# Optimization experiments

Hardware: AMD Instinct MI355X
Metric: run time of the kernel (lower is better)

Reference implementation:

```python
import jax, jax.numpy as jnp
import numpy as np

IN_FEATURES = 4096
OUT_FEATURES = 4096
PACKED_IN = (IN_FEATURES + 3) // 4  # 1024


def _unpack_ternary(packed, scale, original_in_features):
    # packed: (O, P) uint8; each byte holds 4 two-bit fields encoding {-1,0,+1} as {0,1,2}
    p = packed.astype(jnp.uint8)
    fields = jnp.stack(
        [p & 3, (p >> 2) & 3, (p >> 4) & 3, (p >> 6) & 3], axis=-1
    )  # (O, P, 4)
    unpacked = fields.reshape(packed.shape[0], -1)[:, :original_in_features]
    decoded = unpacked.astype(scale.dtype) - 1.0  # back to {-1,0,+1}
    return decoded * scale  # per-output-channel scale, (O, IN)


def setup_inputs() -> dict:
    key = jax.random.key(0)
    k_x, k_w, k_s, k_b = jax.random.split(key, 4)
    x = jax.random.normal(k_x, (4, 2048, IN_FEATURES), dtype=jnp.float32)
    # sample ternary codes {0,1,2} per 2-bit field, then pack 4 per byte
    fields = jax.random.randint(k_w, (OUT_FEATURES, PACKED_IN, 4), 0, 3).astype(jnp.uint8)
    packed_weight = (
        fields[..., 0]
        | (fields[..., 1] << 2)
        | (fields[..., 2] << 4)
        | (fields[..., 3] << 6)
    )  # (O, P) uint8
    scale = jax.random.uniform(k_s, (OUT_FEATURES, 1), dtype=jnp.float32, minval=0.01, maxval=0.1)
    bias = jax.random.normal(k_b, (OUT_FEATURES,), dtype=jnp.float32)
    return {"x": x, "packed_weight": packed_weight, "scale": scale, "bias": bias}


def reference(x, packed_weight, scale, bias):
    weight = _unpack_ternary(packed_weight, scale, IN_FEATURES)  # (O, IN) fp32
    # F.linear: x @ W.T + b
    return jnp.einsum("bsi,oi->bso", x, weight) + bias
```

## Files before the change

kernel.cpp:

```cpp
#include <hip/hip_runtime.h>
#include <hip/hip_bf16.h>
#include <stdint.h>

#define M_TOT 8192
#define N_TOT 4096
#define K_TOT 4096
#define PACKED_K 1024

typedef __attribute__((ext_vector_type(4))) float f32x4;
typedef __attribute__((ext_vector_type(4))) int i32x4;
typedef __attribute__((ext_vector_type(16))) int i32x16;
typedef __attribute__((ext_vector_type(4))) unsigned int u32x4;

typedef const __attribute__((address_space(1))) void* gas_cptr;
typedef __attribute__((address_space(3))) void* las_ptr;

#define SX (6.0f / 127.0f)
#define SX_INV (127.0f / 6.0f)

__device__ __forceinline__ void gload_lds16(const void* g, void* l) {
    __builtin_amdgcn_global_load_lds((gas_cptr)g, (las_ptr)l, 16, 0, 0);
}

__global__ void detect_i32(const uint32_t* __restrict__ pw, uint32_t* __restrict__ flag) {
    if (threadIdx.x == 0) {
        uint32_t small = 1u;
        for (int i = 0; i < 64; ++i)
            if (pw[i] > 255u) small = 0u;
        *flag = small;
    }
}


__device__ __forceinline__ uint32_t q8pack(f32x4 v) {
    int a = (int)rintf(fminf(fmaxf(v.x * SX_INV, -127.f), 127.f));
    int b = (int)rintf(fminf(fmaxf(v.y * SX_INV, -127.f), 127.f));
    int c = (int)rintf(fminf(fmaxf(v.z * SX_INV, -127.f), 127.f));
    int d = (int)rintf(fminf(fmaxf(v.w * SX_INV, -127.f), 127.f));
    return (uint32_t)(a & 0xFF) | ((uint32_t)(b & 0xFF) << 8)
         | ((uint32_t)(c & 0xFF) << 16) | ((uint32_t)(d & 0xFF) << 24);
}

__global__ void quant_x_tiled(const float* __restrict__ x,
                              int8_t* __restrict__ aq, int ngran) {
    int stride = gridDim.x * blockDim.x;
    for (int g = blockIdx.x * blockDim.x + threadIdx.x; g < ngran; g += stride) {
        const int mb = g >> 16;
        const int w16 = g & 65535;
        const int kt = w16 >> 10;
        const int w = w16 & 1023;
        const int kstep = w >> 9;
        const int rb = (w >> 6) & 7;
        const int kslot = (w >> 5) & 1;
        const int rl = w & 31;
        const int row = mb * 256 + rb * 32 + rl;
        const int col = kt * 64 + kstep * 32 + kslot * 16;
        const f32x4* src = (const f32x4*)(x + (size_t)row * K_TOT + col);
        uint32_t w0 = q8pack(src[0]);
        uint32_t w1 = q8pack(src[1]);
        uint32_t w2 = q8pack(src[2]);
        uint32_t w3 = q8pack(src[3]);
        *(u32x4*)(aq + (size_t)g * 16) = (u32x4){w0, w1, w2, w3};
    }
}

__global__ void unpack_w_tiled(const uint8_t* __restrict__ pw,
                               int8_t* __restrict__ bq,
                               const uint32_t* __restrict__ flag, int ngran) {
    const uint32_t i32mode = *flag;
    int stride = gridDim.x * blockDim.x;
    for (int g = blockIdx.x * blockDim.x + threadIdx.x; g < ngran; g += stride) {
        const int nb = g >> 16;
        const int w16 = g & 65535;
        const int kt = w16 >> 10;
        const int w = w16 & 1023;
        const int kstep = w >> 9;
        const int rb = (w >> 6) & 7;
        const int kslot = (w >> 5) & 1;
        const int rl = w & 31;
        const int row = nb * 256 + rb * 32 + rl;
        const int pidx = row * PACKED_K + kt * 16 + kstep * 8 + kslot * 4;
        uint32_t p;
        if (i32mode) {
            const uint32_t* p32 = (const uint32_t*)pw;
            uint32_t b0 = p32[pidx + 0] & 0xFFu;
            uint32_t b1 = p32[pidx + 1] & 0xFFu;
            uint32_t b2 = p32[pidx + 2] & 0xFFu;
            uint32_t b3 = p32[pidx + 3] & 0xFFu;
            p = b0 | (b1 << 8) | (b2 << 16) | (b3 << 24);
        } else {
            p = *(const uint32_t*)(pw + pidx);
        }
        uint32_t o[4];
#pragma unroll
        for (int i = 0; i < 4; ++i) {
            uint32_t b = (p >> (8 * i)) & 0xFFu;
            uint32_t f0 = b & 3u, f1 = (b >> 2) & 3u, f2 = (b >> 4) & 3u, f3 = b >> 6;
            o[i] = ((f0 - 1u) & 0xFFu) | (((f1 - 1u) & 0xFFu) << 8)
                 | (((f2 - 1u) & 0xFFu) << 16) | (((f3 - 1u) & 0xFFu) << 24);
        }
        *(u32x4*)(bq + (size_t)g * 16) = (u32x4){o[0], o[1], o[2], o[3]};
    }
}

__global__ __launch_bounds__(512, 2) void gemm_tern_i8(
        const int8_t* __restrict__ Aq,
        const int8_t* __restrict__ Bq,
        const float* __restrict__ scale,
        const float* __restrict__ bias,
        float* __restrict__ out) {
    __shared__ uint8_t lds[65536];
    uint8_t* ldsA = lds;
    uint8_t* ldsB = lds + 32768;

    const int tid  = threadIdx.x;
    const int lane = tid & 63;
    const int wid  = tid >> 6;
    const int wm   = wid >> 2;
    const int wn   = wid & 3;

    const int wg  = blockIdx.x;
    const int cpx = gridDim.x >> 3;
    const int swz = (wg & 7) * cpx + (wg >> 3);
    const int mblk = swz >> 4;
    const int nblk = swz & 15;
    const int m0  = mblk * 256;
    const int n0  = nblk * 256;

    const int8_t* Abase = Aq + (size_t)mblk * 1048576;
    const int8_t* Bbase = Bq + (size_t)nblk * 1048576;

#define STAGE(t, db) do {                                                             \
        const int8_t* sa = Abase + (size_t)(t) * 16384 + (tid << 4);                  \
        const int8_t* sb = Bbase + (size_t)(t) * 16384 + (tid << 4);                  \
        gload_lds16(sa,        ldsA + (db) * 16384 + (tid << 4));                     \
        gload_lds16(sa + 8192, ldsA + (db) * 16384 + 8192 + (tid << 4));              \
        gload_lds16(sb,        ldsB + (db) * 16384 + (tid << 4));                     \
        gload_lds16(sb + 8192, ldsB + (db) * 16384 + 8192 + (tid << 4));              \
    } while (0)

#define RD_A(mf, ks, db) (*(const i32x4*)(ldsA + (db) * 16384 + (ks) * 8192          \
                              + (wm * 4 + (mf)) * 1024 + (lane << 4)))
#define RD_B(nf, ks, db) (*(const i32x4*)(ldsB + (db) * 16384 + (ks) * 8192          \
                              + (wn * 2 + (nf)) * 1024 + (lane << 4)))

#define BAR()        __builtin_amdgcn_s_barrier()
#define SCHEDBAR()   __builtin_amdgcn_sched_barrier(0)
#define WAIT_LGKM6() asm volatile("s_waitcnt lgkmcnt(6)" ::: "memory")
#define WAIT_LGKM0() asm volatile("s_waitcnt lgkmcnt(0)" ::: "memory")
#define WAIT_VM0()   asm volatile("s_waitcnt vmcnt(0)" ::: "memory")

#define MFMA_I8(a, b, c) __builtin_amdgcn_mfma_i32_32x32x32_i8(a, b, c, 0, 0, 0)

#define KTILE(t, DB)                                                                  \
    a0k0 = RD_A(0, 0, DB); a1k0 = RD_A(1, 0, DB);                                     \
    a2k0 = RD_A(2, 0, DB); a3k0 = RD_A(3, 0, DB);                                     \
    b0k0 = RD_B(0, 0, DB); b1k0 = RD_B(1, 0, DB);                                     \
    a0k1 = RD_A(0, 1, DB); a1k1 = RD_A(1, 1, DB);                                     \
    a2k1 = RD_A(2, 1, DB); a3k1 = RD_A(3, 1, DB);                                     \
    b0k1 = RD_B(0, 1, DB); b1k1 = RD_B(1, 1, DB);                                     \
    if ((t) + 1 < NT) STAGE((t) + 1, 1 - (DB));                                       \
    WAIT_LGKM6(); SCHEDBAR();                                                         \
    __builtin_amdgcn_s_setprio(1);                                                    \
    acc00 = MFMA_I8(a0k0, b0k0, acc00);  acc01 = MFMA_I8(a0k0, b1k0, acc01);          \
    acc10 = MFMA_I8(a1k0, b0k0, acc10);  acc11 = MFMA_I8(a1k0, b1k0, acc11);          \
    acc20 = MFMA_I8(a2k0, b0k0, acc20);  acc21 = MFMA_I8(a2k0, b1k0, acc21);          \
    acc30 = MFMA_I8(a3k0, b0k0, acc30);  acc31 = MFMA_I8(a3k0, b1k0, acc31);          \
    __builtin_amdgcn_s_setprio(0);                                                    \
    WAIT_LGKM0(); SCHEDBAR();                                                         \
    __builtin_amdgcn_s_setprio(1);                                                    \
    acc00 = MFMA_I8(a0k1, b0k1, acc00);  acc01 = MFMA_I8(a0k1, b1k1, acc01);          \
    acc10 = MFMA_I8(a1k1, b0k1, acc10);  acc11 = MFMA_I8(a1k1, b1k1, acc11);          \
    acc20 = MFMA_I8(a2k1, b0k1, acc20);  acc21 = MFMA_I8(a2k1, b1k1, acc21);          \
    acc30 = MFMA_I8(a3k1, b0k1, acc30);  acc31 = MFMA_I8(a3k1, b1k1, acc31);          \
    __builtin_amdgcn_s_setprio(0);                                                    \
    WAIT_VM0();                                                                       \
    BAR();

    i32x16 acc00 = {0}, acc01 = {0}, acc10 = {0}, acc11 = {0};
    i32x16 acc20 = {0}, acc21 = {0}, acc30 = {0}, acc31 = {0};
#pragma unroll
    for (int j = 0; j < 16; ++j) {
        acc00[j] = 0; acc01[j] = 0; acc10[j] = 0; acc11[j] = 0;
        acc20[j] = 0; acc21[j] = 0; acc30[j] = 0; acc31[j] = 0;
    }

    const int NT = K_TOT / 64;

    STAGE(0, 0);
    WAIT_VM0();
    BAR();

    i32x4 a0k0, a1k0, a2k0, a3k0, b0k0, b1k0;
    i32x4 a0k1, a1k1, a2k1, a3k1, b0k1, b1k1;

    for (int t = 0; t < NT; t += 2) {
        KTILE(t, 0);
        KTILE(t + 1, 1);
    }

    const int rl    = lane & 31;
    const int rbase = (lane >> 5) << 2;
#pragma unroll
    for (int nf = 0; nf < 2; ++nf) {
        const int col = n0 + wn * 64 + nf * 32 + rl;
        const float fs = SX * scale[col];
        const float bv = bias[col];
#pragma unroll
        for (int mf = 0; mf < 4; ++mf) {
            const i32x16 a = (mf == 0) ? (nf == 0 ? acc00 : acc01)
                           : (mf == 1) ? (nf == 0 ? acc10 : acc11)
                           : (mf == 2) ? (nf == 0 ? acc20 : acc21)
                                       : (nf == 0 ? acc30 : acc31);
#pragma unroll
            for (int j = 0; j < 16; ++j) {
                const int row = m0 + wm * 128 + mf * 32 + (j & 3) + 8 * (j >> 2) + rbase;
                out[(size_t)row * N_TOT + col] = (float)a[j] * fs + bv;
            }
        }
    }
#undef STAGE
#undef RD_A
#undef RD_B
#undef BAR
#undef SCHEDBAR
#undef WAIT_LGKM6
#undef WAIT_LGKM0
#undef WAIT_VM0
#undef MFMA_I8
#undef KTILE
}

__global__ void naive_tern(const float* __restrict__ x,
                           const uint8_t* __restrict__ pw,
                           const float* __restrict__ scale,
                           const float* __restrict__ bias,
                           float* __restrict__ out) {
    const int n = blockIdx.x * blockDim.x + threadIdx.x;
    const int m = blockIdx.y;
    const uint32_t* p32 = (const uint32_t*)pw;
    bool i32mode = true;
    for (int i = 0; i < 64; ++i)
        if (p32[i] > 255u) { i32mode = false; break; }
    const float* xr = x + (size_t)m * K_TOT;
    float acc = 0.f;
    if (i32mode) {
        const uint32_t* wr = p32 + (size_t)n * PACKED_K;
        for (int p = 0; p < PACKED_K; ++p) {
            uint32_t b = wr[p] & 0xFFu;
            acc += xr[4 * p + 0] * (float)((int)(b & 3u) - 1);
            acc += xr[4 * p + 1] * (float)((int)((b >> 2) & 3u) - 1);
            acc += xr[4 * p + 2] * (float)((int)((b >> 4) & 3u) - 1);
            acc += xr[4 * p + 3] * (float)((int)((b >> 6) & 3u) - 1);
        }
    } else {
        const uint8_t* wr = pw + (size_t)n * PACKED_K;
        for (int p = 0; p < PACKED_K; ++p) {
            uint32_t b = wr[p];
            acc += xr[4 * p + 0] * (float)((int)(b & 3u) - 1);
            acc += xr[4 * p + 1] * (float)((int)((b >> 2) & 3u) - 1);
            acc += xr[4 * p + 2] * (float)((int)((b >> 4) & 3u) - 1);
            acc += xr[4 * p + 3] * (float)((int)((b >> 6) & 3u) - 1);
        }
    }
    out[(size_t)m * N_TOT + n] = acc * scale[n] + bias[n];
}

extern "C" void kernel_launch(void* const* d_in, const int* in_sizes, int n_in,
                              void* d_out, int out_size, void* d_ws, size_t ws_size,
                              hipStream_t stream) {
    const float*   x     = (const float*)d_in[0];
    const uint8_t* pw    = (const uint8_t*)d_in[1];
    const float*   scale = (const float*)d_in[2];
    const float*   bias  = (const float*)d_in[3];
    float*         out   = (float*)d_out;

    const size_t A_BYTES = (size_t)M_TOT * K_TOT;
    const size_t B_BYTES = (size_t)N_TOT * K_TOT;
    const size_t NEED    = A_BYTES + B_BYTES + 64;

    if (ws_size >= NEED) {
        int8_t*   Aq   = (int8_t*)d_ws;
        int8_t*   Bq   = (int8_t*)((uint8_t*)d_ws + A_BYTES);
        uint32_t* flag = (uint32_t*)((uint8_t*)d_ws + A_BYTES + B_BYTES);
        detect_i32<<<1, 64, 0, stream>>>((const uint32_t*)pw, flag);
        unpack_w_tiled<<<2048, 256, 0, stream>>>(pw, Bq, flag, (int)(B_BYTES / 16));
        quant_x_tiled<<<2048, 256, 0, stream>>>(x, Aq, (int)(A_BYTES / 16));
        gemm_tern_i8<<<(M_TOT / 256) * (N_TOT / 256), 512, 0, stream>>>(Aq, Bq, scale, bias, out);
    } else {
        dim3 grid(N_TOT / 256, M_TOT);
        naive_tern<<<grid, 256, 0, stream>>>(x, pw, scale, bias, out);
    }
}
```

Baseline: 194.3 us.

## Load B fragments directly from global into registers, keep only A in LDS

The int8 GEMM stops staging the B (weight) tile through LDS. Each wave now loads its B fragments straight from global memory into double-buffered registers one K-tile ahead, which halves LDS use and removes the B LDS reads. The tile traversal is also switched to be N-major with M inner, so neighbouring workgroups share a B block, and the detect kernel uses a wave ballot instead of a serial loop. In exchange, B loads are no longer shared across the two waves that read the same B columns, which doubles B global traffic from L2. Register pressure also rises under launch_bounds(512,2).

```diff
diff --git a/kernel.cpp b/kernel.cpp
--- a/kernel.cpp
+++ b/kernel.cpp
@@ -23,12 +23,8 @@
 }
 
 __global__ void detect_i32(const uint32_t* __restrict__ pw, uint32_t* __restrict__ flag) {
-    if (threadIdx.x == 0) {
-        uint32_t small = 1u;
-        for (int i = 0; i < 64; ++i)
-            if (pw[i] > 255u) small = 0u;
-        *flag = small;
-    }
+    unsigned long long big = __ballot(pw[threadIdx.x & 63] > 255u);
+    if (threadIdx.x == 0) *flag = (big == 0ull) ? 1u : 0u;
 }
 
 
@@ -109,9 +105,7 @@
         const float* __restrict__ scale,
         const float* __restrict__ bias,
         float* __restrict__ out) {
-    __shared__ uint8_t lds[65536];
-    uint8_t* ldsA = lds;
-    uint8_t* ldsB = lds + 32768;
+    __shared__ uint8_t ldsA[32768];
 
     const int tid  = threadIdx.x;
     const int lane = tid & 63;
@@ -122,57 +116,59 @@
     const int wg  = blockIdx.x;
     const int cpx = gridDim.x >> 3;
     const int swz = (wg & 7) * cpx + (wg >> 3);
-    const int mblk = swz >> 4;
-    const int nblk = swz & 15;
+    const int nblk = swz >> 5;
+    const int mblk = swz & 31;
     const int m0  = mblk * 256;
     const int n0  = nblk * 256;
 
     const int8_t* Abase = Aq + (size_t)mblk * 1048576;
     const int8_t* Bbase = Bq + (size_t)nblk * 1048576;
-
-#define STAGE(t, db) do {                                                             \
+    const i32x4*  Bb4   = (const i32x4*)(Bbase + wn * 2048 + (lane << 4));
+
+#define STAGE_A(t, db) do {                                                           \
         const int8_t* sa = Abase + (size_t)(t) * 16384 + (tid << 4);                  \
-        const int8_t* sb = Bbase + (size_t)(t) * 16384 + (tid << 4);                  \
         gload_lds16(sa,        ldsA + (db) * 16384 + (tid << 4));                     \
         gload_lds16(sa + 8192, ldsA + (db) * 16384 + 8192 + (tid << 4));              \
-        gload_lds16(sb,        ldsB + (db) * 16384 + (tid << 4));                     \
-        gload_lds16(sb + 8192, ldsB + (db) * 16384 + 8192 + (tid << 4));              \
+    } while (0)
+
+#define LOADB(r00, r10, r01, r11, t) do {                                             \
+        const i32x4* pb = Bb4 + (size_t)(t) * 1024;                                   \
+        r00 = pb[0]; r10 = pb[64]; r01 = pb[512]; r11 = pb[576];                      \
     } while (0)
 
 #define RD_A(mf, ks, db) (*(const i32x4*)(ldsA + (db) * 16384 + (ks) * 8192          \
                               + (wm * 4 + (mf)) * 1024 + (lane << 4)))
-#define RD_B(nf, ks, db) (*(const i32x4*)(ldsB + (db) * 16384 + (ks) * 8192          \
-                              + (wn * 2 + (nf)) * 1024 + (lane << 4)))
 
 #define BAR()        __builtin_amdgcn_s_barrier()
 #define SCHEDBAR()   __builtin_amdgcn_sched_barrier(0)
-#define WAIT_LGKM6() asm volatile("s_waitcnt lgkmcnt(6)" ::: "memory")
+#define WAIT_LGKM4() asm volatile("s_waitcnt lgkmcnt(4)" ::: "memory")
 #define WAIT_LGKM0() asm volatile("s_waitcnt lgkmcnt(0)" ::: "memory")
 #define WAIT_VM0()   asm volatile("s_waitcnt vmcnt(0)" ::: "memory")
 
 #define MFMA_I8(a, b, c) __builtin_amdgcn_mfma_i32_32x32x32_i8(a, b, c, 0, 0, 0)
 
-#define KTILE(t, DB)                                                                  \
+#define KTILE(t, DB, Bc00, Bc10, Bc01, Bc11, Bn00, Bn10, Bn01, Bn11)                  \
+    if ((t) + 1 < NT) {                                                               \
+        STAGE_A((t) + 1, 1 - (DB));                                                   \
+        LOADB(Bn00, Bn10, Bn01, Bn11, (t) + 1);                                       \
+    }                                                                                 \
     a0k0 = RD_A(0, 0, DB); a1k0 = RD_A(1, 0, DB);                                     \
     a2k0 = RD_A(2, 0, DB); a3k0 = RD_A(3, 0, DB);                                     \
-    b0k0 = RD_B(0, 0, DB); b1k0 = RD_B(1, 0, DB);                                     \
     a0k1 = RD_A(0, 1, DB); a1k1 = RD_A(1, 1, DB);                                     \
     a2k1 = RD_A(2, 1, DB); a3k1 = RD_A(3, 1, DB);                                     \
-    b0k1 = RD_B(0, 1, DB); b1k1 = RD_B(1, 1, DB);                                     \
-    if ((t) + 1 < NT) STAGE((t) + 1, 1 - (DB));                                       \
-    WAIT_LGKM6(); SCHEDBAR();                                                         \
+    WAIT_LGKM4(); SCHEDBAR();                                                         \
     __builtin_amdgcn_s_setprio(1);                                                    \
-    acc00 = MFMA_I8(a0k0, b0k0, acc00);  acc01 = MFMA_I8(a0k0, b1k0, acc01);          \
-    acc10 = MFMA_I8(a1k0, b0k0, acc10);  acc11 = MFMA_I8(a1k0, b1k0, acc11);          \
-    acc20 = MFMA_I8(a2k0, b0k0, acc20);  acc21 = MFMA_I8(a2k0, b1k0, acc21);          \
-    acc30 = MFMA_I8(a3k0, b0k0, acc30);  acc31 = MFMA_I8(a3k0, b1k0, acc31);          \
+    acc00 = MFMA_I8(a0k0, Bc00, acc00);  acc01 = MFMA_I8(a0k0, Bc10, acc01);          \
+    acc10 = MFMA_I8(a1k0, Bc00, acc10);  acc11 = MFMA_I8(a1k0, Bc10, acc11);          \
+    acc20 = MFMA_I8(a2k0, Bc00, acc20);  acc21 = MFMA_I8(a2k0, Bc10, acc21);          \
+    acc30 = MFMA_I8(a3k0, Bc00, acc30);  acc31 = MFMA_I8(a3k0, Bc10, acc31);          \
     __builtin_amdgcn_s_setprio(0);                                                    \
     WAIT_LGKM0(); SCHEDBAR();                                                         \
     __builtin_amdgcn_s_setprio(1);                                                    \
-    acc00 = MFMA_I8(a0k1, b0k1, acc00);  acc01 = MFMA_I8(a0k1, b1k1, acc01);          \
-    acc10 = MFMA_I8(a1k1, b0k1, acc10);  acc11 = MFMA_I8(a1k1, b1k1, acc11);          \
-    acc20 = MFMA_I8(a2k1, b0k1, acc20);  acc21 = MFMA_I8(a2k1, b1k1, acc21);          \
-    acc30 = MFMA_I8(a3k1, b0k1, acc30);  acc31 = MFMA_I8(a3k1, b1k1, acc31);          \
+    acc00 = MFMA_I8(a0k1, Bc01, acc00);  acc01 = MFMA_I8(a0k1, Bc11, acc01);          \
+    acc10 = MFMA_I8(a1k1, Bc01, acc10);  acc11 = MFMA_I8(a1k1, Bc11, acc11);          \
+    acc20 = MFMA_I8(a2k1, Bc01, acc20);  acc21 = MFMA_I8(a2k1, Bc11, acc21);          \
+    acc30 = MFMA_I8(a3k1, Bc01, acc30);  acc31 = MFMA_I8(a3k1, Bc11, acc31);          \
     __builtin_amdgcn_s_setprio(0);                                                    \
     WAIT_VM0();                                                                       \
     BAR();
@@ -187,16 +183,19 @@
 
     const int NT = K_TOT / 64;
 
-    STAGE(0, 0);
+    i32x4 Bx00, Bx10, Bx01, Bx11, By00, By10, By01, By11;
+
+    STAGE_A(0, 0);
+    LOADB(Bx00, Bx10, Bx01, Bx11, 0);
     WAIT_VM0();
     BAR();
 
-    i32x4 a0k0, a1k0, a2k0, a3k0, b0k0, b1k0;
-    i32x4 a0k1, a1k1, a2k1, a3k1, b0k1, b1k1;
+    i32x4 a0k0, a1k0, a2k0, a3k0;
+    i32x4 a0k1, a1k1, a2k1, a3k1;
 
     for (int t = 0; t < NT; t += 2) {
-        KTILE(t, 0);
-        KTILE(t + 1, 1);
+        KTILE(t,     0, Bx00, Bx10, Bx01, Bx11, By00, By10, By01, By11);
+        KTILE(t + 1, 1, By00, By10, By01, By11, Bx00, Bx10, Bx01, Bx11);
     }
 
     const int rl    = lane & 31;
@@ -219,12 +218,12 @@
             }
         }
     }
-#undef STAGE
+#undef STAGE_A
+#undef LOADB
 #undef RD_A
-#undef RD_B
 #undef BAR
 #undef SCHEDBAR
-#undef WAIT_LGKM6
+#undef WAIT_LGKM4
 #undef WAIT_LGKM0
 #undef WAIT_VM0
 #undef MFMA_I8
```

New measurement: 210.9 us. 8.6% more time.

## Deepen int8 GEMM LDS pipeline to four stages with prefetch three tiles ahead

Applied to the files above, without the earlier changes.

The int8 ternary GEMM moves from a double-buffered LDS scheme to a four-slot ring of 32KB tiles. Global-to-LDS loads are issued three K-tiles ahead, and the wait only drains to vmcnt(8), so two tiles stay in flight instead of stalling on every load each iteration. The K loop is unrolled by four with a hand-written tail that stops staging and shrinks the wait counts. This doubles LDS per block to 128KB, which likely limits the CU to one resident 512-thread block instead of the two the launch bounds target, trading occupancy for deeper prefetch. A small secondary change replaces the serial 64-element check in detect_i32 with a wavefront ballot.

```diff
diff --git a/kernel.cpp b/kernel.cpp
--- a/kernel.cpp
+++ b/kernel.cpp
@@ -23,12 +23,8 @@
 }
 
 __global__ void detect_i32(const uint32_t* __restrict__ pw, uint32_t* __restrict__ flag) {
-    if (threadIdx.x == 0) {
-        uint32_t small = 1u;
-        for (int i = 0; i < 64; ++i)
-            if (pw[i] > 255u) small = 0u;
-        *flag = small;
-    }
+    unsigned long long big = __ballot(pw[threadIdx.x & 63] > 255u);
+    if (threadIdx.x == 0) *flag = (big == 0ull) ? 1u : 0u;
 }
 
 
@@ -109,9 +105,7 @@
         const float* __restrict__ scale,
         const float* __restrict__ bias,
         float* __restrict__ out) {
-    __shared__ uint8_t lds[65536];
-    uint8_t* ldsA = lds;
-    uint8_t* ldsB = lds + 32768;
+    __shared__ uint8_t lds[131072];
 
     const int tid  = threadIdx.x;
     const int lane = tid & 63;
@@ -133,48 +127,48 @@
 #define STAGE(t, db) do {                                                             \
         const int8_t* sa = Abase + (size_t)(t) * 16384 + (tid << 4);                  \
         const int8_t* sb = Bbase + (size_t)(t) * 16384 + (tid << 4);                  \
-        gload_lds16(sa,        ldsA + (db) * 16384 + (tid << 4));                     \
-        gload_lds16(sa + 8192, ldsA + (db) * 16384 + 8192 + (tid << 4));              \
-        gload_lds16(sb,        ldsB + (db) * 16384 + (tid << 4));                     \
-        gload_lds16(sb + 8192, ldsB + (db) * 16384 + 8192 + (tid << 4));              \
+        uint8_t* la = lds + (db) * 32768 + (tid << 4);                                \
+        gload_lds16(sa,        la);                                                   \
+        gload_lds16(sa + 8192, la + 8192);                                            \
+        gload_lds16(sb,        la + 16384);                                           \
+        gload_lds16(sb + 8192, la + 24576);                                           \
     } while (0)
 
-#define RD_A(mf, ks, db) (*(const i32x4*)(ldsA + (db) * 16384 + (ks) * 8192          \
+#define RD_A(mf, ks, db) (*(const i32x4*)(lds + (db) * 32768 + (ks) * 8192           \
                               + (wm * 4 + (mf)) * 1024 + (lane << 4)))
-#define RD_B(nf, ks, db) (*(const i32x4*)(ldsB + (db) * 16384 + (ks) * 8192          \
+#define RD_B(nf, ks, db) (*(const i32x4*)(lds + (db) * 32768 + 16384 + (ks) * 8192   \
                               + (wn * 2 + (nf)) * 1024 + (lane << 4)))
 
 #define BAR()        __builtin_amdgcn_s_barrier()
 #define SCHEDBAR()   __builtin_amdgcn_sched_barrier(0)
-#define WAIT_LGKM6() asm volatile("s_waitcnt lgkmcnt(6)" ::: "memory")
-#define WAIT_LGKM0() asm volatile("s_waitcnt lgkmcnt(0)" ::: "memory")
-#define WAIT_VM0()   asm volatile("s_waitcnt vmcnt(0)" ::: "memory")
+#define WAIT_LGKM(N) asm volatile("s_waitcnt lgkmcnt(" #N ")" ::: "memory")
+#define WAIT_VM(N)   asm volatile("s_waitcnt vmcnt(" #N ")" ::: "memory")
 
 #define MFMA_I8(a, b, c) __builtin_amdgcn_mfma_i32_32x32x32_i8(a, b, c, 0, 0, 0)
 
-#define KTILE(t, DB)                                                                  \
+#define KTILE(t, DB, SDB, DO_STAGE, VMC)                                              \
     a0k0 = RD_A(0, 0, DB); a1k0 = RD_A(1, 0, DB);                                     \
     a2k0 = RD_A(2, 0, DB); a3k0 = RD_A(3, 0, DB);                                     \
     b0k0 = RD_B(0, 0, DB); b1k0 = RD_B(1, 0, DB);                                     \
     a0k1 = RD_A(0, 1, DB); a1k1 = RD_A(1, 1, DB);                                     \
     a2k1 = RD_A(2, 1, DB); a3k1 = RD_A(3, 1, DB);                                     \
     b0k1 = RD_B(0, 1, DB); b1k1 = RD_B(1, 1, DB);                                     \
-    if ((t) + 1 < NT) STAGE((t) + 1, 1 - (DB));                                       \
-    WAIT_LGKM6(); SCHEDBAR();                                                         \
+    if (DO_STAGE) STAGE((t) + 3, SDB);                                                \
+    WAIT_LGKM(6); SCHEDBAR();                                                         \
     __builtin_amdgcn_s_setprio(1);                                                    \
     acc00 = MFMA_I8(a0k0, b0k0, acc00);  acc01 = MFMA_I8(a0k0, b1k0, acc01);          \
     acc10 = MFMA_I8(a1k0, b0k0, acc10);  acc11 = MFMA_I8(a1k0, b1k0, acc11);          \
     acc20 = MFMA_I8(a2k0, b0k0, acc20);  acc21 = MFMA_I8(a2k0, b1k0, acc21);          \
     acc30 = MFMA_I8(a3k0, b0k0, acc30);  acc31 = MFMA_I8(a3k0, b1k0, acc31);          \
     __builtin_amdgcn_s_setprio(0);                                                    \
-    WAIT_LGKM0(); SCHEDBAR();                                                         \
+    WAIT_LGKM(0); SCHEDBAR();                                                         \
     __builtin_amdgcn_s_setprio(1);                                                    \
     acc00 = MFMA_I8(a0k1, b0k1, acc00);  acc01 = MFMA_I8(a0k1, b1k1, acc01);          \
     acc10 = MFMA_I8(a1k1, b0k1, acc10);  acc11 = MFMA_I8(a1k1, b1k1, acc11);          \
     acc20 = MFMA_I8(a2k1, b0k1, acc20);  acc21 = MFMA_I8(a2k1, b1k1, acc21);          \
     acc30 = MFMA_I8(a3k1, b0k1, acc30);  acc31 = MFMA_I8(a3k1, b1k1, acc31);          \
     __builtin_amdgcn_s_setprio(0);                                                    \
-    WAIT_VM0();                                                                       \
+    WAIT_VM(VMC); SCHEDBAR();                                                         \
     BAR();
 
     i32x16 acc00 = {0}, acc01 = {0}, acc10 = {0}, acc11 = {0};
@@ -188,16 +182,24 @@
     const int NT = K_TOT / 64;
 
     STAGE(0, 0);
-    WAIT_VM0();
+    STAGE(1, 1);
+    STAGE(2, 2);
+    WAIT_VM(8); SCHEDBAR();
     BAR();
 
     i32x4 a0k0, a1k0, a2k0, a3k0, b0k0, b1k0;
     i32x4 a0k1, a1k1, a2k1, a3k1, b0k1, b1k1;
 
-    for (int t = 0; t < NT; t += 2) {
-        KTILE(t, 0);
-        KTILE(t + 1, 1);
-    }
+    for (int t = 0; t < 60; t += 4) {
+        KTILE(t,     0, 3, 1, 8);
+        KTILE(t + 1, 1, 0, 1, 8);
+        KTILE(t + 2, 2, 1, 1, 8);
+        KTILE(t + 3, 3, 2, 1, 8);
+    }
+    KTILE(60, 0, 3, 1, 8);
+    KTILE(61, 1, 0, 0, 4);
+    KTILE(62, 2, 1, 0, 0);
+    KTILE(63, 3, 2, 0, 0);
 
     const int rl    = lane & 31;
     const int rbase = (lane >> 5) << 2;
@@ -224,9 +226,8 @@
 #undef RD_B
 #undef BAR
 #undef SCHEDBAR
-#undef WAIT_LGKM6
-#undef WAIT_LGKM0
-#undef WAIT_VM0
+#undef WAIT_LGKM
+#undef WAIT_VM
 #undef MFMA_I8
 #undef KTILE
 }
```

After: 190.9 us. About the same (-1.7%).
